# Kernel tuning notes

Hardware: AMD Instinct MI355X
Metric: run time of the kernel (lower is better)

The kernel has to match this reference:

```python
import jax, jax.numpy as jnp
import numpy as np

jax.config.update("jax_enable_x64", True)

MAX_LEN = 2048
D_MODEL = 2048
CONTEXT = 1
FUDGE = 0.01
MIN_PERIOD = 1
MAX_PERIOD = 1024
FORGOTTEN_AT = 0.01


def _init_params():
    # Mirrors LaplaceAggregation.__init__ with init_method='linspace', modify_real=True
    limit = np.log(np.finfo(np.float64).max) / MAX_LEN - FUDGE
    soft_high = np.log(FORGOTTEN_AT) / MAX_PERIOD
    soft_low = np.log(FORGOTTEN_AT) / MIN_PERIOD
    a_low = max(-limit + FUDGE, soft_low)
    a_high = max(min(-1e-6, soft_high), a_low)
    a = np.linspace(a_low, a_high, D_MODEL).reshape(1, 1, D_MODEL, CONTEXT)
    b = (2.0 * np.pi / np.linspace(MIN_PERIOD, MAX_PERIOD, D_MODEL)).reshape(1, 1, D_MODEL, CONTEXT)
    return jnp.asarray(a, jnp.float64), jnp.asarray(b, jnp.float64)


def setup_inputs() -> dict:
    key = jax.random.key(0)
    k1, k2, k3 = jax.random.split(key, 3)
    B, T, F = 8, 1024, D_MODEL
    x = jax.random.normal(k1, (B, T, F), dtype=jnp.float32)
    mem_real = jax.random.normal(k2, (B, 1, F, CONTEXT), dtype=jnp.float32)
    mem_imag = jax.random.normal(k3, (B, 1, F, CONTEXT), dtype=jnp.float32)
    a, b = _init_params()
    return {"x": x, "mem_real": mem_real, "mem_imag": mem_imag, "a": a, "b": b}


def reference(x, mem_real, mem_imag, a, b):
    # batched_recurrent_update path (1 < T < max_len)
    T = x.shape[1]
    f64, c128 = jnp.float64, jnp.complex128
    ab = a.astype(f64) + 1j * b.astype(f64)           # [1,1,F,C] complex

    def psi(t):  # t: [T] -> [1,T,F,C]
        return jnp.exp(ab * t.reshape(1, -1, 1, 1))

    # inner_idx[:T] = [max_len-1, ..., max_len-T]; outer_idx = -inner_idx
    inner = jnp.arange(MAX_LEN - 1, MAX_LEN - 1 - T, -1, dtype=f64)
    offset = jnp.arange(1, T + 1, dtype=f64)          # state_offset[:T]

    xc = x.astype(f64)[..., None].astype(c128)        # [B,T,F,1]
    z = jnp.cumsum(psi(inner) * xc, axis=1)           # [B,T,F,C]
    mem0 = (mem_real.astype(f64) + 1j * mem_imag.astype(f64))  # [B,1,F,C]
    out = psi(-inner) * z + mem0 * psi(offset)        # [B,T,F,C]
    return out.astype(jnp.complex64)
```

## Files before the change

### kernel.cpp

```cpp
#include <hip/hip_runtime.h>
#include <math.h>

#define BB 8
#define TT 1024
#define FF 2048
#define F2 1024
#define LOG2F2 10
#define NC 16
#define LCH (TT / NC)


__device__ inline void load_ab2(const void* ap, const void* bp, int f,
                                double2& ab0, double2& ab1) {
    double bd = ((const double*)bp)[0];
    if (bd > 6.0 && bd < 6.6) {
        ab0 = make_double2(((const double*)ap)[f],     ((const double*)bp)[f]);
        ab1 = make_double2(((const double*)ap)[f + 1], ((const double*)bp)[f + 1]);
    } else {
        ab0 = make_double2((double)((const float*)ap)[f],
                           (double)((const float*)bp)[f]);
        ab1 = make_double2((double)((const float*)ap)[f + 1],
                           (double)((const float*)bp)[f + 1]);
    }
}

__device__ inline float2 cis_exp_f(double a, double b, double scale) {
    double m = exp(scale * a);
    double s, c;
    sincos(scale * b, &s, &c);
    return make_float2((float)(m * c), (float)(m * s));
}

__global__ void __launch_bounds__(256)
k_chunk_sum(const float2* __restrict__ x2, const void* __restrict__ a,
            const void* __restrict__ b, float4* __restrict__ S) {
    int tid = blockIdx.x * blockDim.x + threadIdx.x;
    int f2 = tid & (F2 - 1);
    int bc = tid >> LOG2F2;
    int c  = bc & (NC - 1);
    int bb = bc >> 4;
    double2 ab0, ab1;
    load_ab2(a, b, 2 * f2, ab0, ab1);
    float2 l0 = cis_exp_f(ab0.x, ab0.y, 1.0);
    float2 l1 = cis_exp_f(ab1.x, ab1.y, 1.0);
    const float2* xp = x2 + ((size_t)bb * TT + (size_t)c * LCH) * F2 + f2;
    float wr0 = 0.f, wi0 = 0.f, wr1 = 0.f, wi1 = 0.f;
#pragma unroll 8
    for (int j = 0; j < LCH; ++j) {
        float2 xv = xp[(size_t)j * F2];
        float nr0 = fmaf(l0.x, wr0, fmaf(-l0.y, wi0, xv.x));
        float ni0 = fmaf(l0.x, wi0, l0.y * wr0);
        float nr1 = fmaf(l1.x, wr1, fmaf(-l1.y, wi1, xv.y));
        float ni1 = fmaf(l1.x, wi1, l1.y * wr1);
        wr0 = nr0; wi0 = ni0; wr1 = nr1; wi1 = ni1;
    }
    S[tid] = make_float4(wr0, wi0, wr1, wi1);
}

__global__ void __launch_bounds__(256)
k_scan(const float2* __restrict__ mr2, const float2* __restrict__ mi2,
       const void* __restrict__ a, const void* __restrict__ b,
       float4* __restrict__ S) {
    int tid = blockIdx.x * blockDim.x + threadIdx.x;
    int f2 = tid & (F2 - 1);
    int bb = tid >> LOG2F2;
    double2 ab0, ab1;
    load_ab2(a, b, 2 * f2, ab0, ab1);
    float2 L0 = cis_exp_f(ab0.x, ab0.y, (double)LCH);
    float2 L1 = cis_exp_f(ab1.x, ab1.y, (double)LCH);
    float2 m_r = mr2[tid], m_i = mi2[tid];
    float wr0 = m_r.x, wi0 = m_i.x, wr1 = m_r.y, wi1 = m_i.y;
    float4* Sp = S + (size_t)bb * NC * F2 + f2;
    for (int c = 0; c < NC; ++c) {
        float4 s = Sp[(size_t)c * F2];
        Sp[(size_t)c * F2] = make_float4(wr0, wi0, wr1, wi1);
        float nr0 = fmaf(L0.x, wr0, fmaf(-L0.y, wi0, s.x));
        float ni0 = fmaf(L0.x, wi0, fmaf(L0.y, wr0, s.y));
        float nr1 = fmaf(L1.x, wr1, fmaf(-L1.y, wi1, s.z));
        float ni1 = fmaf(L1.x, wi1, fmaf(L1.y, wr1, s.w));
        wr0 = nr0; wi0 = ni0; wr1 = nr1; wi1 = ni1;
    }
}

__global__ void __launch_bounds__(256)
k_apply(const float2* __restrict__ x2, const void* __restrict__ a,
        const void* __restrict__ b, const float4* __restrict__ S,
        float2* __restrict__ out2, size_t limit2) {
    int tid = blockIdx.x * blockDim.x + threadIdx.x;
    int f2 = tid & (F2 - 1);
    int bc = tid >> LOG2F2;
    int c  = bc & (NC - 1);
    int bb = bc >> 4;
    double2 ab0, ab1;
    load_ab2(a, b, 2 * f2, ab0, ab1);
    float2 l0 = cis_exp_f(ab0.x, ab0.y, 1.0);
    float2 l1 = cis_exp_f(ab1.x, ab1.y, 1.0);
    float4 w0 = S[tid];
    float wr0 = w0.x, wi0 = w0.y, wr1 = w0.z, wi1 = w0.w;
    const size_t plane2 = (size_t)BB * TT * F2;
    size_t base2 = ((size_t)bb * TT + (size_t)c * LCH) * F2 + f2;
    const float2* xp = x2 + base2;
#pragma unroll 8
    for (int j = 0; j < LCH; ++j) {
        float2 xv = xp[(size_t)j * F2];
        float nr0 = fmaf(l0.x, wr0, fmaf(-l0.y, wi0, xv.x));
        float ni0 = fmaf(l0.x, wi0, l0.y * wr0);
        float nr1 = fmaf(l1.x, wr1, fmaf(-l1.y, wi1, xv.y));
        float ni1 = fmaf(l1.x, wi1, l1.y * wr1);
        wr0 = nr0; wi0 = ni0; wr1 = nr1; wi1 = ni1;
        size_t idx2 = base2 + (size_t)j * F2;
        if (idx2 < limit2) out2[idx2] = make_float2(wr0, wr1);
        size_t ii2 = idx2 + plane2;
        if (ii2 < limit2) out2[ii2] = make_float2(wi0, wi1);
    }
}

__global__ void __launch_bounds__(256)
k_single(const float2* __restrict__ x2, const float2* __restrict__ mr2,
         const float2* __restrict__ mi2, const void* __restrict__ a,
         const void* __restrict__ b, float2* __restrict__ out2, size_t limit2) {
    int tid = blockIdx.x * blockDim.x + threadIdx.x;
    int f2 = tid & (F2 - 1);
    int bb = tid >> LOG2F2;
    double2 ab0, ab1;
    load_ab2(a, b, 2 * f2, ab0, ab1);
    float2 l0 = cis_exp_f(ab0.x, ab0.y, 1.0);
    float2 l1 = cis_exp_f(ab1.x, ab1.y, 1.0);
    float2 m_r = mr2[tid], m_i = mi2[tid];
    float wr0 = m_r.x, wi0 = m_i.x, wr1 = m_r.y, wi1 = m_i.y;
    const size_t plane2 = (size_t)BB * TT * F2;
    size_t base2 = (size_t)bb * TT * F2 + f2;
    const float2* xp = x2 + base2;
#pragma unroll 4
    for (int j = 0; j < TT; ++j) {
        float2 xv = xp[(size_t)j * F2];
        float nr0 = fmaf(l0.x, wr0, fmaf(-l0.y, wi0, xv.x));
        float ni0 = fmaf(l0.x, wi0, l0.y * wr0);
        float nr1 = fmaf(l1.x, wr1, fmaf(-l1.y, wi1, xv.y));
        float ni1 = fmaf(l1.x, wi1, l1.y * wr1);
        wr0 = nr0; wi0 = ni0; wr1 = nr1; wi1 = ni1;
        size_t idx2 = base2 + (size_t)j * F2;
        if (idx2 < limit2) out2[idx2] = make_float2(wr0, wr1);
        size_t ii2 = idx2 + plane2;
        if (ii2 < limit2) out2[ii2] = make_float2(wi0, wi1);
    }
}

extern "C" void kernel_launch(void* const* d_in, const int* in_sizes, int n_in,
                              void* d_out, int out_size, void* d_ws, size_t ws_size,
                              hipStream_t stream) {
    const float2* x2  = (const float2*)d_in[0];
    const float2* mr2 = (const float2*)d_in[1];
    const float2* mi2 = (const float2*)d_in[2];
    const void*   a   = d_in[3];
    const void*   b   = d_in[4];
    float2* out2 = (float2*)d_out;

    size_t limit2 = (size_t)out_size >> 1;

    size_t s_bytes = (size_t)BB * NC * F2 * sizeof(float4);
    if (d_ws == nullptr || ws_size < s_bytes) {
        k_single<<<(BB * F2) / 256, 256, 0, stream>>>(x2, mr2, mi2, a, b, out2,
                                                      limit2);
        return;
    }

    float4* S = (float4*)d_ws;
    int nthreads = BB * NC * F2;
    k_chunk_sum<<<nthreads / 256, 256, 0, stream>>>(x2, a, b, S);
    k_scan<<<(BB * F2) / 256, 256, 0, stream>>>(mr2, mi2, a, b, S);
    k_apply<<<nthreads / 256, 256, 0, stream>>>(x2, a, b, S, out2, limit2);
}
```

Baseline: 141.3 us.

## Fuse chunk-sum, scan and apply into one kernel with shared-memory parallel scan

Replaces the three-kernel chunked scan (chunk sums to global workspace, serial scan over chunks, apply pass) with a single kernel where each workgroup holds all 16 time chunks for 32 feature pairs. Chunk carries are combined with a log-step Hillis-Steele scan in shared memory using repeatedly squared decay factors, and memory initial state is added via a per-chunk exp factor. This removes two launches and the global workspace round trip. In exchange it adds block-level barriers and recomputes the transcendental exps per thread, and squaring the decay factor in float may drift slightly in accuracy.

```diff
diff --git a/kernel.cpp b/kernel.cpp
--- a/kernel.cpp
+++ b/kernel.cpp
@@ -5,9 +5,10 @@
 #define TT 1024
 #define FF 2048
 #define F2 1024
-#define LOG2F2 10
-#define NC 16
-#define LCH (TT / NC)
+#define NCH 16
+#define LCH 64
+#define F2W 32
+#define WGT (NCH * F2W)
 
 
 __device__ inline void load_ab2(const void* ap, const void* bp, int f,
@@ -31,108 +32,73 @@
     return make_float2((float)(m * c), (float)(m * s));
 }
 
-__global__ void __launch_bounds__(256)
-k_chunk_sum(const float2* __restrict__ x2, const void* __restrict__ a,
-            const void* __restrict__ b, float4* __restrict__ S) {
-    int tid = blockIdx.x * blockDim.x + threadIdx.x;
-    int f2 = tid & (F2 - 1);
-    int bc = tid >> LOG2F2;
-    int c  = bc & (NC - 1);
-    int bb = bc >> 4;
+__global__ void __launch_bounds__(WGT)
+k_fused(const float2* __restrict__ x2, const float2* __restrict__ mr2,
+        const float2* __restrict__ mi2, const void* __restrict__ a,
+        const void* __restrict__ b, float2* __restrict__ out2, size_t limit2) {
+    __shared__ float4 sS[NCH][F2W];
+
+    int f2 = threadIdx.x & (F2W - 1);
+    int c  = threadIdx.x >> 5;
+    int fb = blockIdx.x & 31;
+    int bb = blockIdx.x >> 5;
+    int f2g = fb * F2W + f2;
+
     double2 ab0, ab1;
-    load_ab2(a, b, 2 * f2, ab0, ab1);
+    load_ab2(a, b, 2 * f2g, ab0, ab1);
     float2 l0 = cis_exp_f(ab0.x, ab0.y, 1.0);
     float2 l1 = cis_exp_f(ab1.x, ab1.y, 1.0);
-    const float2* xp = x2 + ((size_t)bb * TT + (size_t)c * LCH) * F2 + f2;
-    float wr0 = 0.f, wi0 = 0.f, wr1 = 0.f, wi1 = 0.f;
+
+    size_t base2 = ((size_t)bb * TT + (size_t)c * LCH) * F2 + f2g;
+    const float2* xp = x2 + base2;
+
+    float zr0 = 0.f, zi0 = 0.f, zr1 = 0.f, zi1 = 0.f;
 #pragma unroll 8
     for (int j = 0; j < LCH; ++j) {
         float2 xv = xp[(size_t)j * F2];
-        float nr0 = fmaf(l0.x, wr0, fmaf(-l0.y, wi0, xv.x));
-        float ni0 = fmaf(l0.x, wi0, l0.y * wr0);
-        float nr1 = fmaf(l1.x, wr1, fmaf(-l1.y, wi1, xv.y));
-        float ni1 = fmaf(l1.x, wi1, l1.y * wr1);
-        wr0 = nr0; wi0 = ni0; wr1 = nr1; wi1 = ni1;
+        float nr0 = fmaf(l0.x, zr0, fmaf(-l0.y, zi0, xv.x));
+        float ni0 = fmaf(l0.x, zi0, l0.y * zr0);
+        float nr1 = fmaf(l1.x, zr1, fmaf(-l1.y, zi1, xv.y));
+        float ni1 = fmaf(l1.x, zi1, l1.y * zr1);
+        zr0 = nr0; zi0 = ni0; zr1 = nr1; zi1 = ni1;
     }
-    S[tid] = make_float4(wr0, wi0, wr1, wi1);
-}
+    sS[c][f2] = make_float4(zr0, zi0, zr1, zi1);
+    __syncthreads();
 
-__global__ void __launch_bounds__(256)
-k_scan(const float2* __restrict__ mr2, const float2* __restrict__ mi2,
-       const void* __restrict__ a, const void* __restrict__ b,
-       float4* __restrict__ S) {
-    int tid = blockIdx.x * blockDim.x + threadIdx.x;
-    int f2 = tid & (F2 - 1);
-    int bb = tid >> LOG2F2;
-    double2 ab0, ab1;
-    load_ab2(a, b, 2 * f2, ab0, ab1);
-    float2 L0 = cis_exp_f(ab0.x, ab0.y, (double)LCH);
-    float2 L1 = cis_exp_f(ab1.x, ab1.y, (double)LCH);
-    float2 m_r = mr2[tid], m_i = mi2[tid];
-    float wr0 = m_r.x, wi0 = m_i.x, wr1 = m_r.y, wi1 = m_i.y;
-    float4* Sp = S + (size_t)bb * NC * F2 + f2;
-    for (int c = 0; c < NC; ++c) {
-        float4 s = Sp[(size_t)c * F2];
-        Sp[(size_t)c * F2] = make_float4(wr0, wi0, wr1, wi1);
-        float nr0 = fmaf(L0.x, wr0, fmaf(-L0.y, wi0, s.x));
-        float ni0 = fmaf(L0.x, wi0, fmaf(L0.y, wr0, s.y));
-        float nr1 = fmaf(L1.x, wr1, fmaf(-L1.y, wi1, s.z));
-        float ni1 = fmaf(L1.x, wi1, fmaf(L1.y, wr1, s.w));
-        wr0 = nr0; wi0 = ni0; wr1 = nr1; wi1 = ni1;
+    float2 m0 = cis_exp_f(ab0.x, ab0.y, (double)LCH);
+    float2 m1 = cis_exp_f(ab1.x, ab1.y, (double)LCH);
+    float4 P = sS[c][f2];
+#pragma unroll
+    for (int r = 0; r < 4; ++r) {
+        int k = 1 << r;
+        float4 part = make_float4(0.f, 0.f, 0.f, 0.f);
+        if (c >= k) part = sS[c - k][f2];
+        __syncthreads();
+        P.x = fmaf(m0.x, part.x, fmaf(-m0.y, part.y, P.x));
+        P.y = fmaf(m0.x, part.y, fmaf( m0.y, part.x, P.y));
+        P.z = fmaf(m1.x, part.z, fmaf(-m1.y, part.w, P.z));
+        P.w = fmaf(m1.x, part.w, fmaf( m1.y, part.z, P.w));
+        sS[c][f2] = P;
+        float2 n0 = make_float2(fmaf(m0.x, m0.x, -m0.y * m0.y), 2.f * m0.x * m0.y);
+        float2 n1 = make_float2(fmaf(m1.x, m1.x, -m1.y * m1.y), 2.f * m1.x * m1.y);
+        m0 = n0; m1 = n1;
+        __syncthreads();
     }
-}
 
-__global__ void __launch_bounds__(256)
-k_apply(const float2* __restrict__ x2, const void* __restrict__ a,
-        const void* __restrict__ b, const float4* __restrict__ S,
-        float2* __restrict__ out2, size_t limit2) {
-    int tid = blockIdx.x * blockDim.x + threadIdx.x;
-    int f2 = tid & (F2 - 1);
-    int bc = tid >> LOG2F2;
-    int c  = bc & (NC - 1);
-    int bb = bc >> 4;
-    double2 ab0, ab1;
-    load_ab2(a, b, 2 * f2, ab0, ab1);
-    float2 l0 = cis_exp_f(ab0.x, ab0.y, 1.0);
-    float2 l1 = cis_exp_f(ab1.x, ab1.y, 1.0);
-    float4 w0 = S[tid];
-    float wr0 = w0.x, wi0 = w0.y, wr1 = w0.z, wi1 = w0.w;
+    float4 Pm1 = make_float4(0.f, 0.f, 0.f, 0.f);
+    if (c > 0) Pm1 = sS[c - 1][f2];
+    float2 mem_r = mr2[(size_t)bb * F2 + f2g];
+    float2 mem_i = mi2[(size_t)bb * F2 + f2g];
+    float2 e0 = cis_exp_f(ab0.x, ab0.y, (double)(c * LCH));
+    float2 e1 = cis_exp_f(ab1.x, ab1.y, (double)(c * LCH));
+    float wr0 = fmaf(e0.x, mem_r.x, fmaf(-e0.y, mem_i.x, Pm1.x));
+    float wi0 = fmaf(e0.x, mem_i.x, fmaf( e0.y, mem_r.x, Pm1.y));
+    float wr1 = fmaf(e1.x, mem_r.y, fmaf(-e1.y, mem_i.y, Pm1.z));
+    float wi1 = fmaf(e1.x, mem_i.y, fmaf( e1.y, mem_r.y, Pm1.w));
+
     const size_t plane2 = (size_t)BB * TT * F2;
-    size_t base2 = ((size_t)bb * TT + (size_t)c * LCH) * F2 + f2;
-    const float2* xp = x2 + base2;
 #pragma unroll 8
     for (int j = 0; j < LCH; ++j) {
-        float2 xv = xp[(size_t)j * F2];
-        float nr0 = fmaf(l0.x, wr0, fmaf(-l0.y, wi0, xv.x));
-        float ni0 = fmaf(l0.x, wi0, l0.y * wr0);
-        float nr1 = fmaf(l1.x, wr1, fmaf(-l1.y, wi1, xv.y));
-        float ni1 = fmaf(l1.x, wi1, l1.y * wr1);
-        wr0 = nr0; wi0 = ni0; wr1 = nr1; wi1 = ni1;
-        size_t idx2 = base2 + (size_t)j * F2;
-        if (idx2 < limit2) out2[idx2] = make_float2(wr0, wr1);
-        size_t ii2 = idx2 + plane2;
-        if (ii2 < limit2) out2[ii2] = make_float2(wi0, wi1);
-    }
-}
-
-__global__ void __launch_bounds__(256)
-k_single(const float2* __restrict__ x2, const float2* __restrict__ mr2,
-         const float2* __restrict__ mi2, const void* __restrict__ a,
-         const void* __restrict__ b, float2* __restrict__ out2, size_t limit2) {
-    int tid = blockIdx.x * blockDim.x + threadIdx.x;
-    int f2 = tid & (F2 - 1);
-    int bb = tid >> LOG2F2;
-    double2 ab0, ab1;
-    load_ab2(a, b, 2 * f2, ab0, ab1);
-    float2 l0 = cis_exp_f(ab0.x, ab0.y, 1.0);
-    float2 l1 = cis_exp_f(ab1.x, ab1.y, 1.0);
-    float2 m_r = mr2[tid], m_i = mi2[tid];
-    float wr0 = m_r.x, wi0 = m_i.x, wr1 = m_r.y, wi1 = m_i.y;
-    const size_t plane2 = (size_t)BB * TT * F2;
-    size_t base2 = (size_t)bb * TT * F2 + f2;
-    const float2* xp = x2 + base2;
-#pragma unroll 4
-    for (int j = 0; j < TT; ++j) {
         float2 xv = xp[(size_t)j * F2];
         float nr0 = fmaf(l0.x, wr0, fmaf(-l0.y, wi0, xv.x));
         float ni0 = fmaf(l0.x, wi0, l0.y * wr0);
@@ -155,19 +121,10 @@
     const void*   a   = d_in[3];
     const void*   b   = d_in[4];
     float2* out2 = (float2*)d_out;
+    (void)d_ws; (void)ws_size; (void)n_in; (void)in_sizes;
 
     size_t limit2 = (size_t)out_size >> 1;
 
-    size_t s_bytes = (size_t)BB * NC * F2 * sizeof(float4);
-    if (d_ws == nullptr || ws_size < s_bytes) {
-        k_single<<<(BB * F2) / 256, 256, 0, stream>>>(x2, mr2, mi2, a, b, out2,
-                                                      limit2);
-        return;
-    }
-
-    float4* S = (float4*)d_ws;
-    int nthreads = BB * NC * F2;
-    k_chunk_sum<<<nthreads / 256, 256, 0, stream>>>(x2, a, b, S);
-    k_scan<<<(BB * F2) / 256, 256, 0, stream>>>(mr2, mi2, a, b, S);
-    k_apply<<<nthreads / 256, 256, 0, stream>>>(x2, a, b, S, out2, limit2);
+    int grid = BB * (FF / (2 * F2W));
+    k_fused<<<grid, WGT, 0, stream>>>(x2, mr2, mi2, a, b, out2, limit2);
 }
```

After: 137.1 us. 1.03x faster.
